# Performance work log

Measured on AMD Instinct MI355X. Metric: run time of the kernel, lower is better.

Reference implementation:

```python
import jax, jax.numpy as jnp
import numpy as np

D_MODEL = 2048
NUM_HEADS = 16
THETA = 10000.0


def _rope_tables(seq_len, d_k, theta):
    inv_freqs = 1.0 / theta ** (jnp.arange(0, d_k, 2, dtype=jnp.float32) / d_k)
    pos = jnp.arange(seq_len, dtype=jnp.float32)
    ang = jnp.outer(pos, inv_freqs)  # [S, d_k/2]
    return jnp.cos(ang), jnp.sin(ang)


def _apply_rope(x, cos, sin):
    # x: [B, H, S, d_k]; cos/sin: [S, d_k/2]
    x_even, x_odd = x[..., 0::2], x[..., 1::2]
    r_even = x_even * cos - x_odd * sin
    r_odd = x_even * sin + x_odd * cos
    # interleave back: stack on last axis then flatten pairs
    return jnp.stack([r_even, r_odd], axis=-1).reshape(x.shape)


def setup_inputs() -> dict:
    key = jax.random.key(0)
    k1, k2, k3 = jax.random.split(key, 3)
    B, S, D = 4, 2048, D_MODEL
    std_qkv = np.sqrt(2.0 / (D + 3 * D))
    std_out = np.sqrt(2.0 / (D + D))
    x = jax.random.normal(k1, (B, S, D), dtype=jnp.float32)
    w_qkv = jax.random.normal(k2, (3 * D, D), dtype=jnp.float32) * std_qkv
    w_out = jax.random.normal(k3, (D, D), dtype=jnp.float32) * std_out
    return {"x": x, "w_qkv": w_qkv, "w_out": w_out}


def reference(x, w_qkv, w_out):
    B, S, D = x.shape
    H = NUM_HEADS
    d_k = D // H

    # fused QKV projection: Linear stores weight [d_out, d_in]
    qkv = jnp.einsum('bsd,ed->bse', x, w_qkv)            # [B, S, 3*D]
    qkv = qkv.reshape(B, S, 3, H, d_k)
    q = jnp.transpose(qkv[:, :, 0], (0, 2, 1, 3))        # [B, H, S, d_k]
    k = jnp.transpose(qkv[:, :, 1], (0, 2, 1, 3))
    v = jnp.transpose(qkv[:, :, 2], (0, 2, 1, 3))

    cos, sin = _rope_tables(S, d_k, THETA)
    q = _apply_rope(q, cos, sin)
    k = _apply_rope(k, cos, sin)

    scale = 1.0 / jnp.sqrt(jnp.asarray(d_k, dtype=x.dtype))
    scores = jnp.einsum('bhqd,bhkd->bhqk', q, k) * scale  # [B, H, S, S]
    causal = jnp.tril(jnp.ones((S, S), dtype=bool))
    scores = jnp.where(causal, scores, -jnp.inf)
    attn = jax.nn.softmax(scores, axis=-1)
    out = jnp.einsum('bhqk,bhkd->bhqd', attn, v)          # [B, H, S, d_k]
    out = jnp.transpose(out, (0, 2, 1, 3)).reshape(B, S, D)
    return jnp.einsum('bsd,ed->bse', out, w_out)          # output proj
```

## Files before the change

### kernel.cpp

```cpp
#include <hip/hip_runtime.h>
#include <hip/hip_bf16.h>
#include <math.h>

typedef __hip_bfloat16 bf16;
typedef __attribute__((ext_vector_type(8))) short short8;
typedef __attribute__((ext_vector_type(4))) float floatx4;

constexpr int Bb = 4, Ss = 2048, Dd = 2048, Hh = 16, DKk = 128;

__device__ __forceinline__ void async_ld16(const bf16* g, bf16* l) {
    __builtin_amdgcn_global_load_lds(
        (__attribute__((address_space(1))) void*)g,
        (__attribute__((address_space(3))) void*)l, 16, 0, 0);
}

__device__ __forceinline__ unsigned int pk2(float a, float b) {
    bf16 ha = __float2bfloat16(a), hb = __float2bfloat16(b);
    unsigned short ua, ub;
    __builtin_memcpy(&ua, &ha, 2);
    __builtin_memcpy(&ub, &hb, 2);
    return (unsigned int)ua | ((unsigned int)ub << 16);
}

__global__ void prep(const float* __restrict__ x, const float* __restrict__ wq,
                     const float* __restrict__ wo,
                     bf16* __restrict__ xb, bf16* __restrict__ wqb,
                     bf16* __restrict__ wob, float2* __restrict__ rt) {
    const int gb = blockIdx.x;
    if (gb < 16384) {
        const float* in; bf16* out; int i;
        if (gb < 8192)       { in = x;  out = xb;  i = gb * 256 + threadIdx.x; }
        else if (gb < 14336) { in = wq; out = wqb; i = (gb - 8192) * 256 + threadIdx.x; }
        else                 { in = wo; out = wob; i = (gb - 14336) * 256 + threadIdx.x; }
        const float4* p = (const float4*)in + 2 * (size_t)i;
        float4 a = p[0], b = p[1];
        float v[8] = {a.x, a.y, a.z, a.w, b.x, b.y, b.z, b.w};
        bf16 h[8];
#pragma unroll
        for (int j = 0; j < 8; j++) h[j] = __float2bfloat16(v[j]);
        __builtin_memcpy(out + 8 * (size_t)i, h, 16);
    } else {
        int i = (gb - 16384) * 256 + threadIdx.x;
        int s = i >> 6, f = i & 63;
        float inv_freq = powf(10000.0f, -(float)(2 * f) / 128.0f);
        float ang = (float)s * inv_freq;
        rt[i] = make_float2(cosf(ang), sinf(ang));
    }
}

template <int EPI>
__global__ __launch_bounds__(256, 2)
void gemm_bf16(const bf16* __restrict__ A, const bf16* __restrict__ Bm,
               int N, int K,
               float* __restrict__ outF,
               bf16* __restrict__ qb, bf16* __restrict__ kb, bf16* __restrict__ vtb,
               const float2* __restrict__ rope) {
    __shared__ bf16 As[128 * 64];
    __shared__ bf16 Bs[128 * 64];
    const int tid = threadIdx.x;
    const int wave = tid >> 6, lane = tid & 63;
    const int quad = lane >> 4, l16 = lane & 15;
    const int wm = wave >> 1, wn = wave & 1;
    const int m0 = blockIdx.y * 128;
    const int n0 = blockIdx.x * 128;

    const int srow = tid >> 3;
    const int schunk = (tid & 7) ^ (srow & 7);
    const bf16* apr[4];
    const bf16* bpr[4];
#pragma unroll
    for (int r = 0; r < 4; r++) {
        apr[r] = A  + (size_t)(m0 + r * 32 + srow) * K + schunk * 8;
        bpr[r] = Bm + (size_t)(n0 + r * 32 + srow) * K + schunk * 8;
    }
    bf16* asd = As + tid * 8;
    bf16* bsd = Bs + tid * 8;

    floatx4 acc[4][4] = {};
    const int swz = l16 & 7;

    for (int k0 = 0; k0 < K; k0 += 64) {
        __syncthreads();
#pragma unroll
        for (int r = 0; r < 4; r++) {
            async_ld16(apr[r] + k0, asd + r * 2048);
            async_ld16(bpr[r] + k0, bsd + r * 2048);
        }
        __syncthreads();
#pragma unroll
        for (int kk = 0; kk < 2; kk++) {
            short8 af[4], bfr[4];
#pragma unroll
            for (int i = 0; i < 4; i++)
                af[i] = *(const short8*)(As + (wm * 64 + i * 16 + l16) * 64 + (((kk * 4 + quad) ^ swz) * 8));
#pragma unroll
            for (int j = 0; j < 4; j++)
                bfr[j] = *(const short8*)(Bs + (wn * 64 + j * 16 + l16) * 64 + (((kk * 4 + quad) ^ swz) * 8));
#pragma unroll
            for (int i = 0; i < 4; i++)
#pragma unroll
                for (int j = 0; j < 4; j++)
                    acc[i][j] = __builtin_amdgcn_mfma_f32_16x16x32_bf16(af[i], bfr[j], acc[i][j], 0, 0, 0);
        }
    }

    if (EPI == 0) {
#pragma unroll
        for (int i = 0; i < 4; i++) {
            const int gm0 = m0 + wm * 64 + i * 16 + quad * 4;
#pragma unroll
            for (int j = 0; j < 4; j++) {
                const int gn = n0 + wn * 64 + j * 16 + l16;
#pragma unroll
                for (int r = 0; r < 4; r++)
                    outF[(size_t)(gm0 + r) * N + gn] = acc[i][j][r];
            }
        }
    } else {
        const int t = n0 >> 11;
        const int h = (n0 >> 7) & 15;
        const float qscale = 0.08838834764831845f * 1.442695040888963f;
        if (t < 2) {
#pragma unroll
            for (int j = 0; j < 4; j++) {
                const int d = wn * 64 + j * 16 + l16;
#pragma unroll
                for (int i = 0; i < 4; i++) {
#pragma unroll
                    for (int r = 0; r < 4; r++) {
                        const int gm = m0 + wm * 64 + i * 16 + quad * 4 + r;
                        const int b = gm >> 11, s = gm & 2047;
                        const size_t bh = (size_t)(b * Hh + h);
                        float val = acc[i][j][r];
                        float partner = __shfl_xor(val, 1, 64);
                        float2 cs = rope[s * 64 + (d >> 1)];
                        float nv = (d & 1) ? (val * cs.x + partner * cs.y)
                                           : (val * cs.x - partner * cs.y);
                        if (t == 0) {
                            qb[(bh * Ss + s) * DKk + d] = __float2bfloat16(nv * qscale);
                        } else {
                            kb[(bh * Ss + s) * DKk + d] = __float2bfloat16(nv);
                        }
                    }
                }
            }
        } else {
#pragma unroll
            for (int j = 0; j < 4; j++) {
                const int d = wn * 64 + j * 16 + l16;
#pragma unroll
                for (int i = 0; i < 4; i++) {
                    const int gm = m0 + wm * 64 + i * 16 + quad * 4;
                    const int b = gm >> 11, s = gm & 2047;
                    const size_t bh = (size_t)(b * Hh + h);
                    unsigned int w[2];
                    w[0] = pk2(acc[i][j][0], acc[i][j][1]);
                    w[1] = pk2(acc[i][j][2], acc[i][j][3]);
                    __builtin_memcpy(vtb + (bh * DKk + d) * Ss + s, w, 8);
                }
            }
        }
    }
}

template <bool DIAG>
__device__ __forceinline__ void attn_tile(
    int c0, int qw0,
    const bf16* __restrict__ kbp, const bf16* __restrict__ vbp,
    bf16* Ks, bf16* Vs,
    const short8 (&qB)[2][4],
    floatx4 (&oacc)[8][2], float (&m_i)[2], float (&l_i)[2],
    int tid, int wave, int quad, int l16, int srow, int chunkg, int swz)
{
    __syncthreads();
#pragma unroll
    for (int r = 0; r < 8; r++) {
        async_ld16(kbp + (size_t)(c0 + r * 16 + srow) * DKk + chunkg * 8,
                   Ks + ((r * 256 + tid) << 3));
        async_ld16(vbp + (size_t)(r * 16 + srow) * Ss + c0 + chunkg * 8,
                   Vs + ((r * 256 + tid) << 3));
    }
    __syncthreads();

    const int lim_n = DIAG ? (wave * 2 + 2) : 8;
    const int lim_k = DIAG ? (wave + 1) : 4;

    floatx4 sf[8][2];
#pragma unroll
    for (int n = 0; n < 8; n++) {
        if (n < lim_n) {
            short8 kf[4];
#pragma unroll
            for (int kk = 0; kk < 4; kk++)
                kf[kk] = *(const short8*)(Ks + (n * 16 + l16) * 128 + (((kk * 4 + quad) ^ swz) * 8));
            sf[n][0] = (floatx4){0.f, 0.f, 0.f, 0.f};
            sf[n][1] = (floatx4){0.f, 0.f, 0.f, 0.f};
#pragma unroll
            for (int kk = 0; kk < 4; kk++) {
                sf[n][0] = __builtin_amdgcn_mfma_f32_16x16x32_bf16(kf[kk], qB[0][kk], sf[n][0], 0, 0, 0);
                sf[n][1] = __builtin_amdgcn_mfma_f32_16x16x32_bf16(kf[kk], qB[1][kk], sf[n][1], 0, 0, 0);
            }
        }
    }

    unsigned int pp01[8][2], pp23[8][2];
#pragma unroll
    for (int qf = 0; qf < 2; qf++) {
        float mx = -__builtin_inff();
        if (DIAG) {
            const int qrow = qw0 + qf * 16 + l16;
#pragma unroll
            for (int n = 0; n < 8; n++) {
                if (n < lim_n) {
                    const int kvb = c0 + n * 16 + quad * 4;
#pragma unroll
                    for (int r = 0; r < 4; r++) {
                        float v = sf[n][qf][r];
                        v = (kvb + r > qrow) ? -__builtin_inff() : v;
                        sf[n][qf][r] = v;
                        mx = fmaxf(mx, v);
                    }
                }
            }
        } else {
#pragma unroll
            for (int n = 0; n < 8; n++)
#pragma unroll
                for (int r = 0; r < 4; r++) mx = fmaxf(mx, sf[n][qf][r]);
        }
        mx = fmaxf(mx, __shfl_xor(mx, 16, 64));
        mx = fmaxf(mx, __shfl_xor(mx, 32, 64));
        const float mnew = fmaxf(m_i[qf], mx);
        const float alpha = __builtin_amdgcn_exp2f(m_i[qf] - mnew);
        m_i[qf] = mnew;
        float rs = 0.f;
#pragma unroll
        for (int n = 0; n < 8; n++) {
            if (n < lim_n) {
                float p0 = __builtin_amdgcn_exp2f(sf[n][qf][0] - mnew);
                float p1 = __builtin_amdgcn_exp2f(sf[n][qf][1] - mnew);
                float p2 = __builtin_amdgcn_exp2f(sf[n][qf][2] - mnew);
                float p3 = __builtin_amdgcn_exp2f(sf[n][qf][3] - mnew);
                rs += (p0 + p1) + (p2 + p3);
                pp01[n][qf] = pk2(p0, p1);
                pp23[n][qf] = pk2(p2, p3);
            }
        }
        rs += __shfl_xor(rs, 16, 64);
        rs += __shfl_xor(rs, 32, 64);
        l_i[qf] = l_i[qf] * alpha + rs;
#pragma unroll
        for (int md = 0; md < 8; md++)
#pragma unroll
            for (int r = 0; r < 4; r++) oacc[md][qf][r] *= alpha;
    }

    const int srcA = ((quad & 1) * 2) * 16 + l16;
    const int srcB = srcA + 16;
#pragma unroll
    for (int kv = 0; kv < 4; kv++) {
        if (kv < lim_k) {
            short8 pB[2];
#pragma unroll
            for (int qf = 0; qf < 2; qf++) {
                unsigned int a01 = (unsigned int)__shfl((int)pp01[2 * kv][qf], srcA, 64);
                unsigned int a23 = (unsigned int)__shfl((int)pp23[2 * kv][qf], srcA, 64);
                unsigned int a45 = (unsigned int)__shfl((int)pp01[2 * kv][qf], srcB, 64);
                unsigned int a67 = (unsigned int)__shfl((int)pp23[2 * kv][qf], srcB, 64);
                unsigned int b01 = (unsigned int)__shfl((int)pp01[2 * kv + 1][qf], srcA, 64);
                unsigned int b23 = (unsigned int)__shfl((int)pp23[2 * kv + 1][qf], srcA, 64);
                unsigned int b45 = (unsigned int)__shfl((int)pp01[2 * kv + 1][qf], srcB, 64);
                unsigned int b67 = (unsigned int)__shfl((int)pp23[2 * kv + 1][qf], srcB, 64);
                const bool hi = quad >= 2;
                unsigned int e[4];
                e[0] = hi ? b01 : a01;
                e[1] = hi ? b23 : a23;
                e[2] = hi ? b45 : a45;
                e[3] = hi ? b67 : a67;
                __builtin_memcpy(&pB[qf], e, 16);
            }
#pragma unroll
            for (int md = 0; md < 8; md++) {
                short8 vf = *(const short8*)(Vs + (md * 16 + l16) * 128 + (((kv * 4 + quad) ^ swz) * 8));
                oacc[md][0] = __builtin_amdgcn_mfma_f32_16x16x32_bf16(vf, pB[0], oacc[md][0], 0, 0, 0);
                oacc[md][1] = __builtin_amdgcn_mfma_f32_16x16x32_bf16(vf, pB[1], oacc[md][1], 0, 0, 0);
            }
        }
    }
}

__global__ __launch_bounds__(256, 2)
void flash_attn(const bf16* __restrict__ q, const bf16* __restrict__ k,
                const bf16* __restrict__ vt, bf16* __restrict__ o) {
    __shared__ bf16 Ks[128 * 128];
    __shared__ bf16 Vs[128 * 128];
    const int tid = threadIdx.x, wave = tid >> 6, lane = tid & 63;
    const int quad = lane >> 4, l16 = lane & 15;
    const int bh = blockIdx.y;
    const int xp = blockIdx.x;
    const bf16* qbp = q  + (size_t)bh * Ss * DKk;
    const bf16* kbp = k  + (size_t)bh * Ss * DKk;
    const bf16* vbp = vt + (size_t)bh * DKk * Ss;
    const int b = bh >> 4, h = bh & 15;

    const int srow = tid >> 4;
    const int chunkg = (tid & 15) ^ (srow & 7);
    const int swz = (l16 & 7);

    for (int pass = 0; pass < 2; ++pass) {
        const int xq = pass ? xp : 15 - xp;
        const int qw0 = xq * 128 + wave * 32;

        short8 qB[2][4];
#pragma unroll
        for (int qf = 0; qf < 2; qf++)
#pragma unroll
            for (int kk = 0; kk < 4; kk++)
                qB[qf][kk] = *(const short8*)(qbp + (size_t)(qw0 + qf * 16 + l16) * DKk + kk * 32 + quad * 8);

        floatx4 oacc[8][2] = {};
        float m_i[2] = {-__builtin_inff(), -__builtin_inff()};
        float l_i[2] = {0.f, 0.f};

        for (int it = 0; it < xq; ++it)
            attn_tile<false>(it * 128, qw0, kbp, vbp, Ks, Vs, qB, oacc, m_i, l_i,
                             tid, wave, quad, l16, srow, chunkg, swz);
        attn_tile<true>(xq * 128, qw0, kbp, vbp, Ks, Vs, qB, oacc, m_i, l_i,
                        tid, wave, quad, l16, srow, chunkg, swz);

#pragma unroll
        for (int qf = 0; qf < 2; qf++) {
            const float inv = 1.0f / l_i[qf];
            const int s = qw0 + qf * 16 + l16;
            bf16* orow = o + (size_t)(b * Ss + s) * Dd + h * 128;
#pragma unroll
            for (int md = 0; md < 8; md++) {
                unsigned int w[2];
                w[0] = pk2(oacc[md][qf][0] * inv, oacc[md][qf][1] * inv);
                w[1] = pk2(oacc[md][qf][2] * inv, oacc[md][qf][3] * inv);
                __builtin_memcpy(orow + md * 16 + quad * 4, w, 8);
            }
        }
    }
}

extern "C" void kernel_launch(void* const* d_in, const int* in_sizes, int n_in,
                              void* d_out, int out_size, void* d_ws, size_t ws_size,
                              hipStream_t stream) {
    const float* x     = (const float*)d_in[0];
    const float* w_qkv = (const float*)d_in[1];
    const float* w_out = (const float*)d_in[2];
    float* out = (float*)d_out;
    char* ws = (char*)d_ws;

    bf16*   xb  = (bf16*)(ws);
    bf16*   wqb = (bf16*)(ws + 33554432);
    bf16*   wob = (bf16*)(ws + 58720256);
    bf16*   qb  = (bf16*)(ws + 67108864);
    bf16*   kb  = (bf16*)(ws + 100663296);
    bf16*   vtb = (bf16*)(ws + 134217728);
    float2* rt  = (float2*)(ws + 167772160);

    prep<<<16896, 256, 0, stream>>>(x, w_qkv, w_out, xb, wqb, wob, rt);

    gemm_bf16<1><<<dim3(48, 64), 256, 0, stream>>>(xb, wqb, 6144, 2048,
                                                   nullptr, qb, kb, vtb, rt);
    flash_attn<<<dim3(8, 64), 256, 0, stream>>>(qb, kb, vtb, xb);
    gemm_bf16<0><<<dim3(16, 64), 256, 0, stream>>>(xb, wob, 2048, 2048,
                                                   out, nullptr, nullptr, nullptr, rt);
}
```

Measured before the change: 527.5 us.

## Replace 128x128 GEMM with double-buffered 256x256 tile, 8-wave pipelined kernel

Both projection GEMMs now use 256x256 output tiles with 8 waves per block instead of 128x128 with 4 waves. LDS tiles are double-buffered, and the loads for the next K step are issued in halves between MFMA phases, with barriers, setprio and partial vmcnt waits so memory traffic overlaps compute. The larger tile raises reuse of each loaded operand and cuts global loads. The costs are 128KB of LDS per block, fewer blocks (256 for the output GEMM, fewer than two per CU), and a hand-written schedule that depends on exact wait counts.

```diff
diff --git a/kernel.cpp b/kernel.cpp
--- a/kernel.cpp
+++ b/kernel.cpp
@@ -7,6 +7,7 @@
 typedef __attribute__((ext_vector_type(4))) float floatx4;
 
 constexpr int Bb = 4, Ss = 2048, Dd = 2048, Hh = 16, DKk = 128;
+constexpr int KK = 2048, NTt = 32;
 
 __device__ __forceinline__ void async_ld16(const bf16* g, bf16* l) {
     __builtin_amdgcn_global_load_lds(
@@ -48,66 +49,127 @@
     }
 }
 
+__device__ __forceinline__ void stage_half(const bf16* __restrict__ src,
+                                           bf16* __restrict__ dst, int tid) {
+#pragma unroll
+    for (int c = 0; c < 2; c++) {
+        const int idx = c * 512 + tid;
+        const int row = idx >> 3;
+        const int sch = (idx & 7) ^ (row & 7);
+        async_ld16(src + (size_t)row * KK + sch * 8, dst + idx * 8);
+    }
+}
+
 template <int EPI>
-__global__ __launch_bounds__(256, 2)
-void gemm_bf16(const bf16* __restrict__ A, const bf16* __restrict__ Bm,
-               int N, int K,
-               float* __restrict__ outF,
-               bf16* __restrict__ qb, bf16* __restrict__ kb, bf16* __restrict__ vtb,
-               const float2* __restrict__ rope) {
-    __shared__ bf16 As[128 * 64];
-    __shared__ bf16 Bs[128 * 64];
+__global__ __launch_bounds__(512, 2)
+void gemm256(const bf16* __restrict__ A, const bf16* __restrict__ Bm, int N,
+             float* __restrict__ outF,
+             bf16* __restrict__ qb, bf16* __restrict__ kb, bf16* __restrict__ vtb,
+             const float2* __restrict__ rope) {
+    __shared__ bf16 As[2][256 * 64];
+    __shared__ bf16 Bs[2][256 * 64];
     const int tid = threadIdx.x;
     const int wave = tid >> 6, lane = tid & 63;
     const int quad = lane >> 4, l16 = lane & 15;
-    const int wm = wave >> 1, wn = wave & 1;
-    const int m0 = blockIdx.y * 128;
-    const int n0 = blockIdx.x * 128;
-
-    const int srow = tid >> 3;
-    const int schunk = (tid & 7) ^ (srow & 7);
-    const bf16* apr[4];
-    const bf16* bpr[4];
-#pragma unroll
-    for (int r = 0; r < 4; r++) {
-        apr[r] = A  + (size_t)(m0 + r * 32 + srow) * K + schunk * 8;
-        bpr[r] = Bm + (size_t)(n0 + r * 32 + srow) * K + schunk * 8;
-    }
-    bf16* asd = As + tid * 8;
-    bf16* bsd = Bs + tid * 8;
-
-    floatx4 acc[4][4] = {};
+    const int wm = wave >> 2, wn = wave & 3;
+    const int m0 = blockIdx.y * 256;
+    const int n0 = blockIdx.x * 256;
     const int swz = l16 & 7;
 
-    for (int k0 = 0; k0 < K; k0 += 64) {
-        __syncthreads();
-#pragma unroll
-        for (int r = 0; r < 4; r++) {
-            async_ld16(apr[r] + k0, asd + r * 2048);
-            async_ld16(bpr[r] + k0, bsd + r * 2048);
-        }
-        __syncthreads();
-#pragma unroll
-        for (int kk = 0; kk < 2; kk++) {
-            short8 af[4], bfr[4];
-#pragma unroll
-            for (int i = 0; i < 4; i++)
-                af[i] = *(const short8*)(As + (wm * 64 + i * 16 + l16) * 64 + (((kk * 4 + quad) ^ swz) * 8));
+    const bf16* Arow = A  + (size_t)m0 * KK;
+    const bf16* Brow = Bm + (size_t)n0 * KK;
+
+    floatx4 acc[8][4] = {};
+
+    stage_half(Arow,                         &As[0][0],    tid);
+    stage_half(Arow + (size_t)128 * KK,      &As[0][8192], tid);
+    stage_half(Brow,                         &Bs[0][0],    tid);
+    stage_half(Brow + (size_t)128 * KK,      &Bs[0][8192], tid);
+    stage_half(Arow + 64,                    &As[1][0],    tid);
+    stage_half(Arow + (size_t)128 * KK + 64, &As[1][8192], tid);
+    asm volatile("s_waitcnt vmcnt(4)" ::: "memory");
+    __builtin_amdgcn_s_barrier();
+    __builtin_amdgcn_sched_barrier(0);
+
+    auto tile = [&](int t, bf16* Ac, bf16* Bc, bf16* An2, bf16* Bn2) {
+        short8 aF[4][2], bF[4][2];
+#pragma unroll
+        for (int i = 0; i < 4; i++)
+#pragma unroll
+            for (int kk = 0; kk < 2; kk++)
+                aF[i][kk] = *(const short8*)(Ac + (wm * 128 + i * 16 + l16) * 64 + (((kk * 4 + quad) ^ swz) * 8));
+#pragma unroll
+        for (int j = 0; j < 4; j++)
+            bF[j][0] = *(const short8*)(Bc + (wn * 64 + j * 16 + l16) * 64 + ((quad ^ swz) * 8));
+        if (t + 1 < NTt)
+            stage_half(Brow + (t + 1) * 64, Bn2, tid);
+        __builtin_amdgcn_s_barrier(); __builtin_amdgcn_sched_barrier(0);
+        __builtin_amdgcn_s_setprio(1);
+#pragma unroll
+        for (int i = 0; i < 4; i++)
 #pragma unroll
             for (int j = 0; j < 4; j++)
-                bfr[j] = *(const short8*)(Bs + (wn * 64 + j * 16 + l16) * 64 + (((kk * 4 + quad) ^ swz) * 8));
-#pragma unroll
-            for (int i = 0; i < 4; i++)
-#pragma unroll
-                for (int j = 0; j < 4; j++)
-                    acc[i][j] = __builtin_amdgcn_mfma_f32_16x16x32_bf16(af[i], bfr[j], acc[i][j], 0, 0, 0);
-        }
+                acc[i][j] = __builtin_amdgcn_mfma_f32_16x16x32_bf16(aF[i][0], bF[j][0], acc[i][j], 0, 0, 0);
+        __builtin_amdgcn_s_setprio(0);
+        __builtin_amdgcn_s_barrier(); __builtin_amdgcn_sched_barrier(0);
+
+#pragma unroll
+        for (int j = 0; j < 4; j++)
+            bF[j][1] = *(const short8*)(Bc + (wn * 64 + j * 16 + l16) * 64 + (((4 + quad) ^ swz) * 8));
+        if (t + 1 < NTt)
+            stage_half(Brow + (size_t)128 * KK + (t + 1) * 64, Bn2 + 8192, tid);
+        __builtin_amdgcn_s_barrier(); __builtin_amdgcn_sched_barrier(0);
+        __builtin_amdgcn_s_setprio(1);
+#pragma unroll
+        for (int i = 0; i < 4; i++)
+#pragma unroll
+            for (int j = 0; j < 4; j++)
+                acc[i][j] = __builtin_amdgcn_mfma_f32_16x16x32_bf16(aF[i][1], bF[j][1], acc[i][j], 0, 0, 0);
+        __builtin_amdgcn_s_setprio(0);
+        __builtin_amdgcn_s_barrier(); __builtin_amdgcn_sched_barrier(0);
+
+#pragma unroll
+        for (int i = 0; i < 4; i++)
+#pragma unroll
+            for (int kk = 0; kk < 2; kk++)
+                aF[i][kk] = *(const short8*)(Ac + (wm * 128 + 64 + i * 16 + l16) * 64 + (((kk * 4 + quad) ^ swz) * 8));
+        __builtin_amdgcn_s_barrier(); __builtin_amdgcn_sched_barrier(0);
+        __builtin_amdgcn_s_setprio(1);
+#pragma unroll
+        for (int i = 0; i < 4; i++)
+#pragma unroll
+            for (int j = 0; j < 4; j++)
+                acc[4 + i][j] = __builtin_amdgcn_mfma_f32_16x16x32_bf16(aF[i][0], bF[j][0], acc[4 + i][j], 0, 0, 0);
+        __builtin_amdgcn_s_setprio(0);
+        __builtin_amdgcn_s_barrier(); __builtin_amdgcn_sched_barrier(0);
+
+        if (t + 2 < NTt) {
+            stage_half(Arow + (t + 2) * 64,                    Ac,        tid);
+            stage_half(Arow + (size_t)128 * KK + (t + 2) * 64, Ac + 8192, tid);
+        }
+        __builtin_amdgcn_s_barrier(); __builtin_amdgcn_sched_barrier(0);
+        __builtin_amdgcn_s_setprio(1);
+#pragma unroll
+        for (int i = 0; i < 4; i++)
+#pragma unroll
+            for (int j = 0; j < 4; j++)
+                acc[4 + i][j] = __builtin_amdgcn_mfma_f32_16x16x32_bf16(aF[i][1], bF[j][1], acc[4 + i][j], 0, 0, 0);
+        __builtin_amdgcn_s_setprio(0);
+        if (t + 2 < NTt) { asm volatile("s_waitcnt vmcnt(4)" ::: "memory"); }
+        else             { asm volatile("s_waitcnt vmcnt(0)" ::: "memory"); }
+        __builtin_amdgcn_s_barrier(); __builtin_amdgcn_sched_barrier(0);
+    };
+
+#pragma unroll 1
+    for (int t = 0; t < NTt; t += 2) {
+        tile(t,     &As[0][0], &Bs[0][0], &As[1][0], &Bs[1][0]);
+        tile(t + 1, &As[1][0], &Bs[1][0], &As[0][0], &Bs[0][0]);
     }
 
     if (EPI == 0) {
 #pragma unroll
-        for (int i = 0; i < 4; i++) {
-            const int gm0 = m0 + wm * 64 + i * 16 + quad * 4;
+        for (int i = 0; i < 8; i++) {
+            const int gm0 = m0 + wm * 128 + i * 16 + quad * 4;
 #pragma unroll
             for (int j = 0; j < 4; j++) {
                 const int gn = n0 + wn * 64 + j * 16 + l16;
@@ -117,18 +179,18 @@
             }
         }
     } else {
-        const int t = n0 >> 11;
-        const int h = (n0 >> 7) & 15;
+        const int tq = n0 >> 11;
+        const int h = ((n0 >> 7) + (wn >> 1)) & 15;
         const float qscale = 0.08838834764831845f * 1.442695040888963f;
-        if (t < 2) {
+        if (tq < 2) {
 #pragma unroll
             for (int j = 0; j < 4; j++) {
-                const int d = wn * 64 + j * 16 + l16;
-#pragma unroll
-                for (int i = 0; i < 4; i++) {
+                const int d = (wn & 1) * 64 + j * 16 + l16;
+#pragma unroll
+                for (int i = 0; i < 8; i++) {
 #pragma unroll
                     for (int r = 0; r < 4; r++) {
-                        const int gm = m0 + wm * 64 + i * 16 + quad * 4 + r;
+                        const int gm = m0 + wm * 128 + i * 16 + quad * 4 + r;
                         const int b = gm >> 11, s = gm & 2047;
                         const size_t bh = (size_t)(b * Hh + h);
                         float val = acc[i][j][r];
@@ -136,7 +198,7 @@
                         float2 cs = rope[s * 64 + (d >> 1)];
                         float nv = (d & 1) ? (val * cs.x + partner * cs.y)
                                            : (val * cs.x - partner * cs.y);
-                        if (t == 0) {
+                        if (tq == 0) {
                             qb[(bh * Ss + s) * DKk + d] = __float2bfloat16(nv * qscale);
                         } else {
                             kb[(bh * Ss + s) * DKk + d] = __float2bfloat16(nv);
@@ -147,10 +209,10 @@
         } else {
 #pragma unroll
             for (int j = 0; j < 4; j++) {
-                const int d = wn * 64 + j * 16 + l16;
-#pragma unroll
-                for (int i = 0; i < 4; i++) {
-                    const int gm = m0 + wm * 64 + i * 16 + quad * 4;
+                const int d = (wn & 1) * 64 + j * 16 + l16;
+#pragma unroll
+                for (int i = 0; i < 8; i++) {
+                    const int gm = m0 + wm * 128 + i * 16 + quad * 4;
                     const int b = gm >> 11, s = gm & 2047;
                     const size_t bh = (size_t)(b * Hh + h);
                     unsigned int w[2];
@@ -363,9 +425,9 @@
 
     prep<<<16896, 256, 0, stream>>>(x, w_qkv, w_out, xb, wqb, wob, rt);
 
-    gemm_bf16<1><<<dim3(48, 64), 256, 0, stream>>>(xb, wqb, 6144, 2048,
-                                                   nullptr, qb, kb, vtb, rt);
+    gemm256<1><<<dim3(24, 32), 512, 0, stream>>>(xb, wqb, 6144,
+                                                 nullptr, qb, kb, vtb, rt);
     flash_attn<<<dim3(8, 64), 256, 0, stream>>>(qb, kb, vtb, xb);
-    gemm_bf16<0><<<dim3(16, 64), 256, 0, stream>>>(xb, wob, 2048, 2048,
-                                                   out, nullptr, nullptr, nullptr, rt);
-}
+    gemm256<0><<<dim3(8, 32), 512, 0, stream>>>(xb, wob, 2048,
+                                                out, nullptr, nullptr, nullptr, rt);
+}
```

Measured after the change: 570.0 us. 1.08x slower.

## Shrink flash-attention KV tile to 64, one query block per CTA, raise occupancy

Applied to the files above, without the earlier changes.

The flash-attention kernel now streams K/V in 64-row tiles instead of 128, halving LDS use so launch bounds can request 4 blocks per CU. The paired heavy/light query-block pass scheme is replaced by one query block per workgroup on a 16x64 grid. Causal masking is computed per wave from the row offset, so waves skip fully masked sub-tiles. In exchange there are twice as many barriers and tile loads per query block, and load balance across CTAs now depends on the scheduler rather than on the explicit pairing.

```diff
diff --git a/kernel.cpp b/kernel.cpp
--- a/kernel.cpp
+++ b/kernel.cpp
@@ -163,183 +163,166 @@
     }
 }
 
-template <bool DIAG>
-__device__ __forceinline__ void attn_tile(
-    int c0, int qw0,
-    const bf16* __restrict__ kbp, const bf16* __restrict__ vbp,
-    bf16* Ks, bf16* Vs,
-    const short8 (&qB)[2][4],
-    floatx4 (&oacc)[8][2], float (&m_i)[2], float (&l_i)[2],
-    int tid, int wave, int quad, int l16, int srow, int chunkg, int swz)
-{
-    __syncthreads();
-#pragma unroll
-    for (int r = 0; r < 8; r++) {
-        async_ld16(kbp + (size_t)(c0 + r * 16 + srow) * DKk + chunkg * 8,
-                   Ks + ((r * 256 + tid) << 3));
-        async_ld16(vbp + (size_t)(r * 16 + srow) * Ss + c0 + chunkg * 8,
-                   Vs + ((r * 256 + tid) << 3));
-    }
-    __syncthreads();
-
-    const int lim_n = DIAG ? (wave * 2 + 2) : 8;
-    const int lim_k = DIAG ? (wave + 1) : 4;
-
-    floatx4 sf[8][2];
-#pragma unroll
-    for (int n = 0; n < 8; n++) {
-        if (n < lim_n) {
-            short8 kf[4];
-#pragma unroll
-            for (int kk = 0; kk < 4; kk++)
-                kf[kk] = *(const short8*)(Ks + (n * 16 + l16) * 128 + (((kk * 4 + quad) ^ swz) * 8));
-            sf[n][0] = (floatx4){0.f, 0.f, 0.f, 0.f};
-            sf[n][1] = (floatx4){0.f, 0.f, 0.f, 0.f};
-#pragma unroll
-            for (int kk = 0; kk < 4; kk++) {
-                sf[n][0] = __builtin_amdgcn_mfma_f32_16x16x32_bf16(kf[kk], qB[0][kk], sf[n][0], 0, 0, 0);
-                sf[n][1] = __builtin_amdgcn_mfma_f32_16x16x32_bf16(kf[kk], qB[1][kk], sf[n][1], 0, 0, 0);
-            }
-        }
-    }
-
-    unsigned int pp01[8][2], pp23[8][2];
-#pragma unroll
-    for (int qf = 0; qf < 2; qf++) {
-        float mx = -__builtin_inff();
-        if (DIAG) {
-            const int qrow = qw0 + qf * 16 + l16;
-#pragma unroll
-            for (int n = 0; n < 8; n++) {
-                if (n < lim_n) {
-                    const int kvb = c0 + n * 16 + quad * 4;
-#pragma unroll
-                    for (int r = 0; r < 4; r++) {
-                        float v = sf[n][qf][r];
-                        v = (kvb + r > qrow) ? -__builtin_inff() : v;
-                        sf[n][qf][r] = v;
-                        mx = fmaxf(mx, v);
-                    }
-                }
-            }
-        } else {
-#pragma unroll
-            for (int n = 0; n < 8; n++)
-#pragma unroll
-                for (int r = 0; r < 4; r++) mx = fmaxf(mx, sf[n][qf][r]);
-        }
-        mx = fmaxf(mx, __shfl_xor(mx, 16, 64));
-        mx = fmaxf(mx, __shfl_xor(mx, 32, 64));
-        const float mnew = fmaxf(m_i[qf], mx);
-        const float alpha = __builtin_amdgcn_exp2f(m_i[qf] - mnew);
-        m_i[qf] = mnew;
-        float rs = 0.f;
-#pragma unroll
-        for (int n = 0; n < 8; n++) {
-            if (n < lim_n) {
-                float p0 = __builtin_amdgcn_exp2f(sf[n][qf][0] - mnew);
-                float p1 = __builtin_amdgcn_exp2f(sf[n][qf][1] - mnew);
-                float p2 = __builtin_amdgcn_exp2f(sf[n][qf][2] - mnew);
-                float p3 = __builtin_amdgcn_exp2f(sf[n][qf][3] - mnew);
-                rs += (p0 + p1) + (p2 + p3);
-                pp01[n][qf] = pk2(p0, p1);
-                pp23[n][qf] = pk2(p2, p3);
-            }
-        }
-        rs += __shfl_xor(rs, 16, 64);
-        rs += __shfl_xor(rs, 32, 64);
-        l_i[qf] = l_i[qf] * alpha + rs;
-#pragma unroll
-        for (int md = 0; md < 8; md++)
-#pragma unroll
-            for (int r = 0; r < 4; r++) oacc[md][qf][r] *= alpha;
-    }
-
-    const int srcA = ((quad & 1) * 2) * 16 + l16;
-    const int srcB = srcA + 16;
-#pragma unroll
-    for (int kv = 0; kv < 4; kv++) {
-        if (kv < lim_k) {
-            short8 pB[2];
-#pragma unroll
-            for (int qf = 0; qf < 2; qf++) {
-                unsigned int a01 = (unsigned int)__shfl((int)pp01[2 * kv][qf], srcA, 64);
-                unsigned int a23 = (unsigned int)__shfl((int)pp23[2 * kv][qf], srcA, 64);
-                unsigned int a45 = (unsigned int)__shfl((int)pp01[2 * kv][qf], srcB, 64);
-                unsigned int a67 = (unsigned int)__shfl((int)pp23[2 * kv][qf], srcB, 64);
-                unsigned int b01 = (unsigned int)__shfl((int)pp01[2 * kv + 1][qf], srcA, 64);
-                unsigned int b23 = (unsigned int)__shfl((int)pp23[2 * kv + 1][qf], srcA, 64);
-                unsigned int b45 = (unsigned int)__shfl((int)pp01[2 * kv + 1][qf], srcB, 64);
-                unsigned int b67 = (unsigned int)__shfl((int)pp23[2 * kv + 1][qf], srcB, 64);
-                const bool hi = quad >= 2;
-                unsigned int e[4];
-                e[0] = hi ? b01 : a01;
-                e[1] = hi ? b23 : a23;
-                e[2] = hi ? b45 : a45;
-                e[3] = hi ? b67 : a67;
-                __builtin_memcpy(&pB[qf], e, 16);
-            }
-#pragma unroll
-            for (int md = 0; md < 8; md++) {
-                short8 vf = *(const short8*)(Vs + (md * 16 + l16) * 128 + (((kv * 4 + quad) ^ swz) * 8));
-                oacc[md][0] = __builtin_amdgcn_mfma_f32_16x16x32_bf16(vf, pB[0], oacc[md][0], 0, 0, 0);
-                oacc[md][1] = __builtin_amdgcn_mfma_f32_16x16x32_bf16(vf, pB[1], oacc[md][1], 0, 0, 0);
-            }
-        }
-    }
-}
-
-__global__ __launch_bounds__(256, 2)
+__global__ __launch_bounds__(256, 4)
 void flash_attn(const bf16* __restrict__ q, const bf16* __restrict__ k,
                 const bf16* __restrict__ vt, bf16* __restrict__ o) {
-    __shared__ bf16 Ks[128 * 128];
-    __shared__ bf16 Vs[128 * 128];
+    __shared__ bf16 Ks[64 * 128];
+    __shared__ bf16 Vs[128 * 64];
     const int tid = threadIdx.x, wave = tid >> 6, lane = tid & 63;
     const int quad = lane >> 4, l16 = lane & 15;
     const int bh = blockIdx.y;
-    const int xp = blockIdx.x;
+    const int xq = blockIdx.x;
     const bf16* qbp = q  + (size_t)bh * Ss * DKk;
     const bf16* kbp = k  + (size_t)bh * Ss * DKk;
     const bf16* vbp = vt + (size_t)bh * DKk * Ss;
     const int b = bh >> 4, h = bh & 15;
 
-    const int srow = tid >> 4;
-    const int chunkg = (tid & 15) ^ (srow & 7);
-    const int swz = (l16 & 7);
-
-    for (int pass = 0; pass < 2; ++pass) {
-        const int xq = pass ? xp : 15 - xp;
-        const int qw0 = xq * 128 + wave * 32;
-
-        short8 qB[2][4];
-#pragma unroll
-        for (int qf = 0; qf < 2; qf++)
-#pragma unroll
-            for (int kk = 0; kk < 4; kk++)
-                qB[qf][kk] = *(const short8*)(qbp + (size_t)(qw0 + qf * 16 + l16) * DKk + kk * 32 + quad * 8);
-
-        floatx4 oacc[8][2] = {};
-        float m_i[2] = {-__builtin_inff(), -__builtin_inff()};
-        float l_i[2] = {0.f, 0.f};
-
-        for (int it = 0; it < xq; ++it)
-            attn_tile<false>(it * 128, qw0, kbp, vbp, Ks, Vs, qB, oacc, m_i, l_i,
-                             tid, wave, quad, l16, srow, chunkg, swz);
-        attn_tile<true>(xq * 128, qw0, kbp, vbp, Ks, Vs, qB, oacc, m_i, l_i,
-                        tid, wave, quad, l16, srow, chunkg, swz);
-
+    const int srowK = tid >> 4;
+    const int chunkK = (tid & 15) ^ (srowK & 7);
+    const int srowV = tid >> 3;
+    const int chunkV = (tid & 7) ^ (srowV & 7);
+    const int swz = l16 & 7;
+
+    const int qw0 = xq * 128 + wave * 32;
+
+    short8 qB[2][4];
+#pragma unroll
+    for (int qf = 0; qf < 2; qf++)
+#pragma unroll
+        for (int kk = 0; kk < 4; kk++)
+            qB[qf][kk] = *(const short8*)(qbp + (size_t)(qw0 + qf * 16 + l16) * DKk + kk * 32 + quad * 8);
+
+    floatx4 oacc[8][2] = {};
+    float m_i[2] = {-__builtin_inff(), -__builtin_inff()};
+    float l_i[2] = {0.f, 0.f};
+
+    const int ns = 2 * xq + 2;
+    for (int c = 0; c < ns; ++c) {
+        const int c0 = c * 64;
+        __syncthreads();
+#pragma unroll
+        for (int r = 0; r < 4; r++) {
+            async_ld16(kbp + (size_t)(c0 + r * 16 + srowK) * DKk + chunkK * 8,
+                       Ks + ((r * 256 + tid) << 3));
+            async_ld16(vbp + (size_t)(r * 32 + srowV) * Ss + c0 + chunkV * 8,
+                       Vs + ((r * 256 + tid) << 3));
+        }
+        __syncthreads();
+
+        const int rel = qw0 + 31 - c0;
+        const int lim_n = rel < 0 ? 0 : (rel >= 48 ? 4 : ((rel >> 4) + 1));
+        const int nq = (lim_n + 1) & ~1;
+        const int lim_k = nq >> 1;
+        const bool domask = rel < 94;
+
+        floatx4 sf[4][2];
+#pragma unroll
+        for (int n = 0; n < 4; n++) {
+            if (n < nq) {
+                short8 kf[4];
+#pragma unroll
+                for (int kk = 0; kk < 4; kk++)
+                    kf[kk] = *(const short8*)(Ks + (n * 16 + l16) * 128 + (((kk * 4 + quad) ^ swz) * 8));
+                sf[n][0] = (floatx4){0.f, 0.f, 0.f, 0.f};
+                sf[n][1] = (floatx4){0.f, 0.f, 0.f, 0.f};
+#pragma unroll
+                for (int kk = 0; kk < 4; kk++) {
+                    sf[n][0] = __builtin_amdgcn_mfma_f32_16x16x32_bf16(kf[kk], qB[0][kk], sf[n][0], 0, 0, 0);
+                    sf[n][1] = __builtin_amdgcn_mfma_f32_16x16x32_bf16(kf[kk], qB[1][kk], sf[n][1], 0, 0, 0);
+                }
+            }
+        }
+
+        unsigned int pp01[4][2], pp23[4][2];
 #pragma unroll
         for (int qf = 0; qf < 2; qf++) {
-            const float inv = 1.0f / l_i[qf];
-            const int s = qw0 + qf * 16 + l16;
-            bf16* orow = o + (size_t)(b * Ss + s) * Dd + h * 128;
-#pragma unroll
-            for (int md = 0; md < 8; md++) {
-                unsigned int w[2];
-                w[0] = pk2(oacc[md][qf][0] * inv, oacc[md][qf][1] * inv);
-                w[1] = pk2(oacc[md][qf][2] * inv, oacc[md][qf][3] * inv);
-                __builtin_memcpy(orow + md * 16 + quad * 4, w, 8);
-            }
+            float mx = -__builtin_inff();
+            const int qrow = qw0 + qf * 16 + l16;
+#pragma unroll
+            for (int n = 0; n < 4; n++) {
+                if (n < nq) {
+                    const int kvb = c0 + n * 16 + quad * 4;
+#pragma unroll
+                    for (int r = 0; r < 4; r++) {
+                        float v = sf[n][qf][r];
+                        if (domask) v = (kvb + r > qrow) ? -__builtin_inff() : v;
+                        sf[n][qf][r] = v;
+                        mx = fmaxf(mx, v);
+                    }
+                }
+            }
+            mx = fmaxf(mx, __shfl_xor(mx, 16, 64));
+            mx = fmaxf(mx, __shfl_xor(mx, 32, 64));
+            const float mnew = fmaxf(m_i[qf], mx);
+            const float alpha = __builtin_amdgcn_exp2f(m_i[qf] - mnew);
+            m_i[qf] = mnew;
+            float rs = 0.f;
+#pragma unroll
+            for (int n = 0; n < 4; n++) {
+                if (n < nq) {
+                    float p0 = __builtin_amdgcn_exp2f(sf[n][qf][0] - mnew);
+                    float p1 = __builtin_amdgcn_exp2f(sf[n][qf][1] - mnew);
+                    float p2 = __builtin_amdgcn_exp2f(sf[n][qf][2] - mnew);
+                    float p3 = __builtin_amdgcn_exp2f(sf[n][qf][3] - mnew);
+                    rs += (p0 + p1) + (p2 + p3);
+                    pp01[n][qf] = pk2(p0, p1);
+                    pp23[n][qf] = pk2(p2, p3);
+                }
+            }
+            rs += __shfl_xor(rs, 16, 64);
+            rs += __shfl_xor(rs, 32, 64);
+            l_i[qf] = l_i[qf] * alpha + rs;
+#pragma unroll
+            for (int md = 0; md < 8; md++)
+#pragma unroll
+                for (int r = 0; r < 4; r++) oacc[md][qf][r] *= alpha;
+        }
+
+        const int srcA = ((quad & 1) * 2) * 16 + l16;
+        const int srcB = srcA + 16;
+#pragma unroll
+        for (int kv = 0; kv < 2; kv++) {
+            if (kv < lim_k) {
+                short8 pB[2];
+#pragma unroll
+                for (int qf = 0; qf < 2; qf++) {
+                    unsigned int a01 = (unsigned int)__shfl((int)pp01[2 * kv][qf], srcA, 64);
+                    unsigned int a23 = (unsigned int)__shfl((int)pp23[2 * kv][qf], srcA, 64);
+                    unsigned int a45 = (unsigned int)__shfl((int)pp01[2 * kv][qf], srcB, 64);
+                    unsigned int a67 = (unsigned int)__shfl((int)pp23[2 * kv][qf], srcB, 64);
+                    unsigned int b01 = (unsigned int)__shfl((int)pp01[2 * kv + 1][qf], srcA, 64);
+                    unsigned int b23 = (unsigned int)__shfl((int)pp23[2 * kv + 1][qf], srcA, 64);
+                    unsigned int b45 = (unsigned int)__shfl((int)pp01[2 * kv + 1][qf], srcB, 64);
+                    unsigned int b67 = (unsigned int)__shfl((int)pp23[2 * kv + 1][qf], srcB, 64);
+                    const bool hi = quad >= 2;
+                    unsigned int e[4];
+                    e[0] = hi ? b01 : a01;
+                    e[1] = hi ? b23 : a23;
+                    e[2] = hi ? b45 : a45;
+                    e[3] = hi ? b67 : a67;
+                    __builtin_memcpy(&pB[qf], e, 16);
+                }
+#pragma unroll
+                for (int md = 0; md < 8; md++) {
+                    short8 vf = *(const short8*)(Vs + (md * 16 + l16) * 64 + (((kv * 4 + quad) ^ swz) * 8));
+                    oacc[md][0] = __builtin_amdgcn_mfma_f32_16x16x32_bf16(vf, pB[0], oacc[md][0], 0, 0, 0);
+                    oacc[md][1] = __builtin_amdgcn_mfma_f32_16x16x32_bf16(vf, pB[1], oacc[md][1], 0, 0, 0);
+                }
+            }
+        }
+    }
+
+#pragma unroll
+    for (int qf = 0; qf < 2; qf++) {
+        const float inv = 1.0f / l_i[qf];
+        const int s = qw0 + qf * 16 + l16;
+        bf16* orow = o + (size_t)(b * Ss + s) * Dd + h * 128;
+#pragma unroll
+        for (int md = 0; md < 8; md++) {
+            unsigned int w[2];
+            w[0] = pk2(oacc[md][qf][0] * inv, oacc[md][qf][1] * inv);
+            w[1] = pk2(oacc[md][qf][2] * inv, oacc[md][qf][3] * inv);
+            __builtin_memcpy(orow + md * 16 + quad * 4, w, 8);
         }
     }
 }
@@ -365,7 +348,7 @@
 
     gemm_bf16<1><<<dim3(48, 64), 256, 0, stream>>>(xb, wqb, 6144, 2048,
                                                    nullptr, qb, kb, vtb, rt);
-    flash_attn<<<dim3(8, 64), 256, 0, stream>>>(qb, kb, vtb, xb);
+    flash_attn<<<dim3(16, 64), 256, 0, stream>>>(qb, kb, vtb, xb);
     gemm_bf16<0><<<dim3(16, 64), 256, 0, stream>>>(xb, wob, 2048, 2048,
                                                    out, nullptr, nullptr, nullptr, rt);
 }
```

New measurement: 1.080 ms. +104.7%, slower.
